# Performance work log

Hardware: AMD Instinct MI355X
Metric: run time of the kernel (lower is better)

Reference implementation:

```python
import jax, jax.numpy as jnp
import numpy as np

N_NODES = 100000


def _gcn_layer(x, W, b, src, dst, n):
    # PyG GCNConv: x' = D^-1/2 (A+I) D^-1/2 (x W) + b, with self-loops added.
    x = x @ W  # [N, out]
    loop = jnp.arange(n, dtype=src.dtype)
    src_f = jnp.concatenate([src, loop])
    dst_f = jnp.concatenate([dst, loop])
    deg = jax.ops.segment_sum(jnp.ones_like(dst_f, dtype=x.dtype), dst_f, num_segments=n)
    dinv = jnp.where(deg > 0, jax.lax.rsqrt(deg), 0.0)
    norm = dinv[src_f] * dinv[dst_f]  # [E+N]
    msgs = x[src_f] * norm[:, None]   # gather + scale
    out = jax.ops.segment_sum(msgs, dst_f, num_segments=n)
    return out + b


def setup_inputs() -> dict:
    key = jax.random.key(0)
    ks = jax.random.split(key, 16)
    inputFeatures = jax.random.normal(ks[0], (N_NODES, 64), dtype=jnp.float32)
    edge_index = jax.random.randint(ks[1], (2, 1000000), 0, N_NODES, dtype=jnp.int64)

    def lin(k, fan_in, fan_out):
        s = 1.0 / np.sqrt(fan_in)
        return jax.random.uniform(k, (fan_in, fan_out), jnp.float32, -s, s)

    return {
        "inputFeatures": inputFeatures,
        "W1": lin(ks[2], 64, 100), "b1": jnp.zeros((100,), jnp.float32),
        "W2": lin(ks[3], 100, 50), "b2": jnp.zeros((50,), jnp.float32),
        "W3": lin(ks[4], 50, 25), "b3": jnp.zeros((25,), jnp.float32),
        "Wl1": lin(ks[5], 25, 25), "bl1": jnp.zeros((25,), jnp.float32),
        "Wl2": lin(ks[6], 25, 10), "bl2": jnp.zeros((10,), jnp.float32),
        "Wl3": lin(ks[7], 10, 1), "bl3": jnp.zeros((1,), jnp.float32),
        "edge_index": edge_index,
    }


def reference(inputFeatures, W1, b1, W2, b2, W3, b3, Wl1, bl1, Wl2, bl2, Wl3, bl3, edge_index):
    src, dst = edge_index[0], edge_index[1]
    n = inputFeatures.shape[0]
    x = jax.nn.relu(_gcn_layer(inputFeatures, W1, b1, src, dst, n))
    x = jax.nn.relu(_gcn_layer(x, W2, b2, src, dst, n))
    x = jax.nn.relu(_gcn_layer(x, W3, b3, src, dst, n))
    x = jax.nn.relu(x @ Wl1 + bl1)
    x = jax.nn.relu(x @ Wl2 + bl2)
    x = jax.nn.relu(x @ Wl3 + bl3)
    return x  # [N, 1]
```

## Files before the change

kernel.cpp:

```cpp
#include <hip/hip_runtime.h>
#include <hip/hip_fp16.h>
#include <cstdint>

constexpr int BSHIFT = 9;
constexpr int NBUCK  = 256;
constexpr int BUCKET_CAP = 6144;

struct alignas(16) H8 { __half2 a, b, c, d; };
struct alignas(8)  H4 { __half2 a, b; };

typedef _Float16 f16x8 __attribute__((ext_vector_type(8)));
typedef float    f32x4 __attribute__((ext_vector_type(4)));

__device__ __forceinline__ float4 add4(float4 a, float4 b) {
    return make_float4(a.x + b.x, a.y + b.y, a.z + b.z, a.w + b.w);
}
__device__ __forceinline__ float4 mul4s(float4 a, float s) {
    return make_float4(a.x * s, a.y * s, a.z * s, a.w * s);
}
__device__ __forceinline__ void acc_h8(float4& A0, float4& A1, const H8 v, float s) {
    float2 f0 = __half22float2(v.a), f1 = __half22float2(v.b);
    float2 f2 = __half22float2(v.c), f3 = __half22float2(v.d);
    A0.x = fmaf(f0.x, s, A0.x); A0.y = fmaf(f0.y, s, A0.y);
    A0.z = fmaf(f1.x, s, A0.z); A0.w = fmaf(f1.y, s, A0.w);
    A1.x = fmaf(f2.x, s, A1.x); A1.y = fmaf(f2.y, s, A1.y);
    A1.z = fmaf(f3.x, s, A1.z); A1.w = fmaf(f3.y, s, A1.w);
}


constexpr int EPT = 16;
__global__ __launch_bounds__(256) void partition_edges(
    const int* __restrict__ src, const int* __restrict__ dst,
    int* __restrict__ bucketCur, int* __restrict__ pairs, int ne) {
    __shared__ int lcnt[NBUCK];
    __shared__ int lbase[NBUCK];
    int base = blockIdx.x * (256 * EPT);
    if (threadIdx.x < NBUCK) lcnt[threadIdx.x] = 0;
    __syncthreads();
    int2 ed[EPT];
    int  rnk[EPT];
#pragma unroll
    for (int j = 0; j < EPT; ++j) {
        int e = base + j * 256 + threadIdx.x;
        if (e < ne) {
            int d = dst[e];
            ed[j] = make_int2(src[e], d);
            rnk[j] = atomicAdd(&lcnt[d >> BSHIFT], 1);
        } else {
            ed[j].y = -1;
        }
    }
    __syncthreads();
    if (threadIdx.x < NBUCK) {
        int c = lcnt[threadIdx.x];
        lbase[threadIdx.x] = c ? atomicAdd(&bucketCur[threadIdx.x], c) : 0;
    }
    __syncthreads();
#pragma unroll
    for (int j = 0; j < EPT; ++j) {
        if (ed[j].y >= 0) {
            int b = ed[j].y >> BSHIFT;
            int p = lbase[b] + rnk[j];
            if (p < BUCKET_CAP)
                pairs[(size_t)b * BUCKET_CAP + p] =
                    (ed[j].x << BSHIFT) | (ed[j].y & ((1 << BSHIFT) - 1));
        }
    }
}

__global__ void scan_buckets(const int* __restrict__ bucketCnt, int* __restrict__ bucketBase,
                             int* __restrict__ offs, int n, int ne, int nbuckets) {
    __shared__ int tmp[256];
    int c = (threadIdx.x < (unsigned)nbuckets) ? bucketCnt[threadIdx.x] : 0;
    tmp[threadIdx.x] = c;
    __syncthreads();
    for (int off = 1; off < 256; off <<= 1) {
        int t = (threadIdx.x >= (unsigned)off) ? tmp[threadIdx.x - off] : 0;
        __syncthreads();
        tmp[threadIdx.x] += t;
        __syncthreads();
    }
    if (threadIdx.x < (unsigned)nbuckets) bucketBase[threadIdx.x] = tmp[threadIdx.x] - c;
    if (threadIdx.x == 0) offs[n] = ne;
}

__global__ __launch_bounds__(256) void bucket_csr(
    const int* __restrict__ pairs, const int* __restrict__ bucketCnt,
    const int* __restrict__ bucketBase, int* __restrict__ offs,
    float* __restrict__ dinv, int* __restrict__ csr, int n) {
    constexpr int BN = 1 << BSHIFT;
    __shared__ int hist[BN];
    __shared__ int cur[BN];
    __shared__ int tmp[256];
    int b = blockIdx.x;
    int cnt  = bucketCnt[b];
    int base = bucketBase[b];
    const int* pb = pairs + (size_t)b * BUCKET_CAP;
    int nodeLo = b << BSHIFT;

    hist[threadIdx.x] = 0;
    hist[threadIdx.x + 256] = 0;
    __syncthreads();
    for (int e = threadIdx.x; e < cnt; e += 256)
        atomicAdd(&hist[pb[e] & (BN - 1)], 1);
    __syncthreads();

    int l0 = 2 * threadIdx.x, l1 = l0 + 1;
    int h0 = hist[l0], h1 = hist[l1];
    tmp[threadIdx.x] = h0 + h1;
    __syncthreads();
    for (int off = 1; off < 256; off <<= 1) {
        int t = (threadIdx.x >= (unsigned)off) ? tmp[threadIdx.x - off] : 0;
        __syncthreads();
        tmp[threadIdx.x] += t;
        __syncthreads();
    }
    int e0 = tmp[threadIdx.x] - (h0 + h1);
    int e1 = e0 + h0;
    int g0 = nodeLo + l0, g1 = nodeLo + l1;
    if (g0 < n) { offs[g0] = base + e0; dinv[g0] = rsqrtf((float)(h0 + 1)); }
    if (g1 < n) { offs[g1] = base + e1; dinv[g1] = rsqrtf((float)(h1 + 1)); }
    cur[l0] = e0;
    cur[l1] = e1;
    __syncthreads();

    for (int e = threadIdx.x; e < cnt; e += 256) {
        int p = pb[e];
        int pos = atomicAdd(&cur[p & (BN - 1)], 1);
        csr[base + pos] = ((unsigned)p) >> BSHIFT;
    }
}

__global__ void pack_weights(const float* __restrict__ W1, const float* __restrict__ W2,
                             const float* __restrict__ W3,
                             __half* __restrict__ P1, __half* __restrict__ P2,
                             __half* __restrict__ P3) {
    int t = threadIdx.x;
    for (int i = t; i < 7 * 2 * 64 * 8; i += 256) {
        int j = i & 7, lane = (i >> 3) & 63, f = i >> 9;
        int mt = f >> 1, kf = f & 1;
        int k = kf * 32 + (lane >> 4) * 8 + j;
        int m = mt * 16 + (lane & 15);
        P1[i] = __float2half_rn(m < 100 ? W1[k * 100 + m] : 0.0f);
    }
    for (int i = t; i < 4 * 4 * 64 * 8; i += 256) {
        int j = i & 7, lane = (i >> 3) & 63, f = i >> 9;
        int mt = f >> 2, kf = f & 3;
        int k = kf * 32 + (lane >> 4) * 8 + j;
        int m = mt * 16 + (lane & 15);
        P2[i] = __float2half_rn((k < 100 && m < 50) ? W2[k * 50 + m] : 0.0f);
    }
    for (int i = t; i < 2 * 2 * 64 * 8; i += 256) {
        int j = i & 7, lane = (i >> 3) & 63, f = i >> 9;
        int mt = f >> 1, kf = f & 1;
        int k = kf * 32 + (lane >> 4) * 8 + j;
        int m = mt * 16 + (lane & 15);
        P3[i] = __float2half_rn((k < 50 && m < 25) ? W3[k * 25 + m] : 0.0f);
    }
}

__global__ void cvt_scale_f32_f16(const float* __restrict__ x, const float* __restrict__ dinv,
                                  __half* __restrict__ o, int n4) {
    int i = blockIdx.x * blockDim.x + threadIdx.x;
    if (i < n4) {
        float dv = dinv[i >> 4];
        float4 v = ((const float4*)x)[i];
        H4 h;
        h.a = __floats2half2_rn(v.x * dv, v.y * dv);
        h.b = __floats2half2_rn(v.z * dv, v.w * dv);
        ((H4*)o)[i] = h;
    }
}

__global__ __launch_bounds__(256) void agg1_h(
    const __half* __restrict__ s, const int* __restrict__ offs,
    const int* __restrict__ csr, const float* __restrict__ dinv,
    __half* __restrict__ out, int n) {
    int lane = threadIdx.x & 7;
    int node = blockIdx.x * 32 + (threadIdx.x >> 3);
    if (node >= n) return;
    int f0 = lane * 8;
    float dv = dinv[node];

    float4 z = make_float4(0.f, 0.f, 0.f, 0.f);
    float4 a00 = z, a01 = z, a10 = z, a11 = z, a20 = z, a21 = z, a30 = z, a31 = z;
    {
        H8 sv = *(const H8*)&s[(size_t)node * 64 + f0];
        acc_h8(a00, a01, sv, 1.0f);
    }
    int e0 = offs[node], e1 = offs[node + 1];
    int e = e0;
    for (; e + 4 <= e1; e += 4) {
        int i0 = csr[e], i1 = csr[e + 1], i2 = csr[e + 2], i3 = csr[e + 3];
        H8 v0 = *(const H8*)&s[(size_t)i0 * 64 + f0];
        H8 v1 = *(const H8*)&s[(size_t)i1 * 64 + f0];
        H8 v2 = *(const H8*)&s[(size_t)i2 * 64 + f0];
        H8 v3 = *(const H8*)&s[(size_t)i3 * 64 + f0];
        acc_h8(a00, a01, v0, 1.0f);
        acc_h8(a10, a11, v1, 1.0f);
        acc_h8(a20, a21, v2, 1.0f);
        acc_h8(a30, a31, v3, 1.0f);
    }
    for (; e < e1; ++e) {
        int sid = csr[e];
        H8 v = *(const H8*)&s[(size_t)sid * 64 + f0];
        acc_h8(a00, a01, v, 1.0f);
    }
    float4 A0 = add4(add4(a00, a10), add4(a20, a30));
    float4 A1 = add4(add4(a01, a11), add4(a21, a31));
    A0 = mul4s(A0, dv);
    A1 = mul4s(A1, dv);

    H8 h;
    h.a = __floats2half2_rn(A0.x, A0.y);
    h.b = __floats2half2_rn(A0.z, A0.w);
    h.c = __floats2half2_rn(A1.x, A1.y);
    h.d = __floats2half2_rn(A1.z, A1.w);
    *(H8*)&out[(size_t)node * 64 + f0] = h;
}

__global__ __launch_bounds__(256) void agg2_h16(
    const __half* __restrict__ s, const int* __restrict__ offs,
    const int* __restrict__ csr, const float* __restrict__ dinv,
    const float* __restrict__ b, __half* __restrict__ out, int n) {
    constexpr int MH = 50, SH = 64;
    int lane = threadIdx.x & 7;
    int node = blockIdx.x * 32 + (threadIdx.x >> 3);
    if (node >= n) return;
    int f0 = lane * 8;
    H8 zh{};
    if (f0 >= 56) {
        *(H8*)&out[(size_t)node * SH + f0] = zh;
        return;
    }
    float dv = dinv[node];

    float4 z = make_float4(0.f, 0.f, 0.f, 0.f);
    float4 a00 = z, a01 = z, a10 = z, a11 = z, a20 = z, a21 = z, a30 = z, a31 = z;
    {
        H8 sv = *(const H8*)&s[(size_t)node * SH + f0];
        acc_h8(a00, a01, sv, 1.0f);
    }
    int e0 = offs[node], e1 = offs[node + 1];
    int e = e0;
    for (; e + 4 <= e1; e += 4) {
        int i0 = csr[e], i1 = csr[e + 1], i2 = csr[e + 2], i3 = csr[e + 3];
        H8 v0 = *(const H8*)&s[(size_t)i0 * SH + f0];
        H8 v1 = *(const H8*)&s[(size_t)i1 * SH + f0];
        H8 v2 = *(const H8*)&s[(size_t)i2 * SH + f0];
        H8 v3 = *(const H8*)&s[(size_t)i3 * SH + f0];
        acc_h8(a00, a01, v0, 1.0f);
        acc_h8(a10, a11, v1, 1.0f);
        acc_h8(a20, a21, v2, 1.0f);
        acc_h8(a30, a31, v3, 1.0f);
    }
    for (; e < e1; ++e) {
        H8 v = *(const H8*)&s[(size_t)csr[e] * SH + f0];
        acc_h8(a00, a01, v, 1.0f);
    }
    float4 A0 = add4(add4(a00, a10), add4(a20, a30));
    float4 A1 = add4(add4(a01, a11), add4(a21, a31));
    float v[8] = {A0.x, A0.y, A0.z, A0.w, A1.x, A1.y, A1.z, A1.w};
#pragma unroll
    for (int i = 0; i < 8; ++i)
        v[i] = (f0 + i < MH) ? fmaxf(dv * v[i] + b[f0 + i], 0.0f) : 0.0f;
    H8 h;
    h.a = __floats2half2_rn(v[0], v[1]);
    h.b = __floats2half2_rn(v[2], v[3]);
    h.c = __floats2half2_rn(v[4], v[5]);
    h.d = __floats2half2_rn(v[6], v[7]);
    *(H8*)&out[(size_t)node * SH + f0] = h;
}

constexpr int HP = 136;
__global__ __launch_bounds__(256, 4) void gemm12_mfma(
    const __half* __restrict__ x, const __half* __restrict__ P1,
    const float* __restrict__ b1, const __half* __restrict__ P2,
    const float* __restrict__ dinv, __half* __restrict__ out, int n) {
    __shared__ _Float16 Hs[128 * HP];
    int tid = threadIdx.x;
    int lane = tid & 63;
    int w = tid >> 6;
    int lg = lane >> 4;
    int lr = lane & 15;
    int blockBase = blockIdx.x * 128;
    int waveBase  = blockBase + w * 32;

    for (int i = tid; i < 128 * 2; i += 256) {
        f16x8 zz = {};
        *(f16x8*)&Hs[(i >> 1) * HP + 112 + (i & 1) * 8] = zz;
    }

    float b1v[7];
#pragma unroll
    for (int mt = 0; mt < 7; ++mt) {
        int m = mt * 16 + lr;
        b1v[mt] = (m < 100) ? b1[m] : 0.0f;
    }

    const f16x8* P1v = (const f16x8*)P1;
#pragma unroll
    for (int rt = 0; rt < 2; ++rt) {
        int rowG = waveBase + rt * 16 + lr;
        f16x8 a0 = {}, a1 = {};
        if (rowG < n) {
            a0 = *(const f16x8*)&x[(size_t)rowG * 64 + lg * 8];
            a1 = *(const f16x8*)&x[(size_t)rowG * 64 + 32 + lg * 8];
        }
        int hbase = w * 32 + rt * 16;
#pragma unroll
        for (int mt = 0; mt < 7; ++mt) {
            f16x8 w0 = P1v[(mt * 2 + 0) * 64 + lane];
            f16x8 w1 = P1v[(mt * 2 + 1) * 64 + lane];
            f32x4 acc = {};
            acc = __builtin_amdgcn_mfma_f32_16x16x32_f16(a0, w0, acc, 0, 0, 0);
            acc = __builtin_amdgcn_mfma_f32_16x16x32_f16(a1, w1, acc, 0, 0, 0);
            int col = mt * 16 + lr;
#pragma unroll
            for (int i = 0; i < 4; ++i) {
                int rloc = hbase + lg * 4 + i;
                Hs[rloc * HP + col] = (_Float16)fmaxf(acc[i] + b1v[mt], 0.0f);
            }
        }
    }
    __syncthreads();

    const f16x8* P2v = (const f16x8*)P2;
#pragma unroll
    for (int mt = 0; mt < 4; ++mt) {
        f16x8 w0 = P2v[(mt * 4 + 0) * 64 + lane];
        f16x8 w1 = P2v[(mt * 4 + 1) * 64 + lane];
        f16x8 w2 = P2v[(mt * 4 + 2) * 64 + lane];
        f16x8 w3 = P2v[(mt * 4 + 3) * 64 + lane];
#pragma unroll
        for (int rt = 0; rt < 2; ++rt) {
            int lbase = w * 32 + rt * 16;
            const _Float16* hrow = &Hs[(size_t)(lbase + lr) * HP];
            f16x8 a0 = *(const f16x8*)&hrow[lg * 8];
            f16x8 a1 = *(const f16x8*)&hrow[32 + lg * 8];
            f16x8 a2 = *(const f16x8*)&hrow[64 + lg * 8];
            f16x8 a3 = *(const f16x8*)&hrow[96 + lg * 8];
            f32x4 acc = {};
            acc = __builtin_amdgcn_mfma_f32_16x16x32_f16(a0, w0, acc, 0, 0, 0);
            acc = __builtin_amdgcn_mfma_f32_16x16x32_f16(a1, w1, acc, 0, 0, 0);
            acc = __builtin_amdgcn_mfma_f32_16x16x32_f16(a2, w2, acc, 0, 0, 0);
            acc = __builtin_amdgcn_mfma_f32_16x16x32_f16(a3, w3, acc, 0, 0, 0);
            int col = mt * 16 + lr;
#pragma unroll
            for (int i = 0; i < 4; ++i) {
                int node = blockBase + lbase + lg * 4 + i;
                if (node < n)
                    out[(size_t)node * 64 + col] = __float2half_rn(acc[i] * dinv[node]);
            }
        }
    }
}

__global__ __launch_bounds__(256, 4) void gemm3_mfma(
    const __half* __restrict__ x, const __half* __restrict__ P3,
    const float* __restrict__ dinv, __half* __restrict__ out, int n) {
    int tid = threadIdx.x, lane = tid & 63, w = tid >> 6;
    int lg = lane >> 4, lr = lane & 15;
    int waveBase = blockIdx.x * 128 + w * 32;
    const f16x8* P3v = (const f16x8*)P3;
    f16x8 w00 = P3v[0 * 64 + lane], w01 = P3v[1 * 64 + lane];
    f16x8 w10 = P3v[2 * 64 + lane], w11 = P3v[3 * 64 + lane];
#pragma unroll
    for (int rt = 0; rt < 2; ++rt) {
        int rowG = waveBase + rt * 16 + lr;
        f16x8 a0 = {}, a1 = {};
        if (rowG < n) {
            a0 = *(const f16x8*)&x[(size_t)rowG * 64 + lg * 8];
            a1 = *(const f16x8*)&x[(size_t)rowG * 64 + 32 + lg * 8];
        }
#pragma unroll
        for (int mt = 0; mt < 2; ++mt) {
            f32x4 acc = {};
            acc = __builtin_amdgcn_mfma_f32_16x16x32_f16(a0, mt ? w10 : w00, acc, 0, 0, 0);
            acc = __builtin_amdgcn_mfma_f32_16x16x32_f16(a1, mt ? w11 : w01, acc, 0, 0, 0);
            int col = mt * 16 + lr;
#pragma unroll
            for (int i = 0; i < 4; ++i) {
                int node = waveBase + rt * 16 + lg * 4 + i;
                if (node < n)
                    out[(size_t)node * 32 + col] = __float2half_rn(acc[i] * dinv[node]);
            }
        }
    }
}

__global__ __launch_bounds__(256) void agg3_mlp_h(
    const __half* __restrict__ s, const int* __restrict__ offs,
    const int* __restrict__ csr, const float* __restrict__ dinv,
    const float* __restrict__ bg,
    const float* __restrict__ Wl1, const float* __restrict__ bl1,
    const float* __restrict__ Wl2, const float* __restrict__ bl2,
    const float* __restrict__ Wl3, const float* __restrict__ bl3,
    float* __restrict__ out, int n) {
    constexpr int MH = 25, SH = 32, LPN = 4;
    __shared__ float W1s[625], W2s[250], W3s[10], b1s[25], b2s[10];
    __shared__ float accs[64 * 26];
    __shared__ float b3s;

    for (int i = threadIdx.x; i < 625; i += 256) W1s[i] = Wl1[i];
    for (int i = threadIdx.x; i < 250; i += 256) W2s[i] = Wl2[i];
    if (threadIdx.x < 10) { W3s[threadIdx.x] = Wl3[threadIdx.x]; b2s[threadIdx.x] = bl2[threadIdx.x]; }
    if (threadIdx.x < 25) b1s[threadIdx.x] = bl1[threadIdx.x];
    if (threadIdx.x == 0) b3s = bl3[0];

    int lane = threadIdx.x % LPN;
    int nl   = threadIdx.x / LPN;
    int node = blockIdx.x * 64 + nl;
    int f0 = lane * 8;

    if (node < n && f0 < MH) {
        float dv = dinv[node];
        float4 z = make_float4(0.f, 0.f, 0.f, 0.f);
        float4 a00 = z, a01 = z, a10 = z, a11 = z, a20 = z, a21 = z, a30 = z, a31 = z;
        {
            H8 sv = *(const H8*)&s[(size_t)node * SH + f0];
            acc_h8(a00, a01, sv, 1.0f);
        }
        int e0 = offs[node], e1 = offs[node + 1];
        int e = e0;
        for (; e + 4 <= e1; e += 4) {
            int i0 = csr[e], i1 = csr[e + 1], i2 = csr[e + 2], i3 = csr[e + 3];
            H8 v0 = *(const H8*)&s[(size_t)i0 * SH + f0];
            H8 v1 = *(const H8*)&s[(size_t)i1 * SH + f0];
            H8 v2 = *(const H8*)&s[(size_t)i2 * SH + f0];
            H8 v3 = *(const H8*)&s[(size_t)i3 * SH + f0];
            acc_h8(a00, a01, v0, 1.0f);
            acc_h8(a10, a11, v1, 1.0f);
            acc_h8(a20, a21, v2, 1.0f);
            acc_h8(a30, a31, v3, 1.0f);
        }
        for (; e < e1; ++e) {
            H8 v = *(const H8*)&s[(size_t)csr[e] * SH + f0];
            acc_h8(a00, a01, v, 1.0f);
        }
        float4 A0 = add4(add4(a00, a10), add4(a20, a30));
        float4 A1 = add4(add4(a01, a11), add4(a21, a31));
        float v[8] = {A0.x, A0.y, A0.z, A0.w, A1.x, A1.y, A1.z, A1.w};
#pragma unroll
        for (int i = 0; i < 8; ++i)
            if (f0 + i < MH)
                accs[nl * 26 + f0 + i] = fmaxf(dv * v[i] + bg[f0 + i], 0.0f);
    }
    __syncthreads();

    if (threadIdx.x < 64) {
        int nd = blockIdx.x * 64 + threadIdx.x;
        if (nd < n) {
            const float* xr = &accs[threadIdx.x * 26];
            float h1[25];
#pragma unroll
            for (int m = 0; m < 25; ++m) {
                float a = b1s[m];
#pragma unroll
                for (int k = 0; k < 25; ++k) a = fmaf(xr[k], W1s[k * 25 + m], a);
                h1[m] = fmaxf(a, 0.0f);
            }
            float h2[10];
#pragma unroll
            for (int m = 0; m < 10; ++m) {
                float a = b2s[m];
#pragma unroll
                for (int k = 0; k < 25; ++k) a = fmaf(h1[k], W2s[k * 10 + m], a);
                h2[m] = fmaxf(a, 0.0f);
            }
            float a = b3s;
#pragma unroll
            for (int k = 0; k < 10; ++k) a = fmaf(h2[k], W3s[k], a);
            out[nd] = fmaxf(a, 0.0f);
        }
    }
}


extern "C" void kernel_launch(void* const* d_in, const int* in_sizes, int n_in,
                              void* d_out, int out_size, void* d_ws, size_t ws_size,
                              hipStream_t stream) {
    const float* x0  = (const float*)d_in[0];
    const float* W1  = (const float*)d_in[1];
    const float* b1  = (const float*)d_in[2];
    const float* W2  = (const float*)d_in[3];
    const float* b2  = (const float*)d_in[4];
    const float* W3  = (const float*)d_in[5];
    const float* b3  = (const float*)d_in[6];
    const float* Wl1 = (const float*)d_in[7];
    const float* bl1 = (const float*)d_in[8];
    const float* Wl2 = (const float*)d_in[9];
    const float* bl2 = (const float*)d_in[10];
    const float* Wl3 = (const float*)d_in[11];
    const float* bl3 = (const float*)d_in[12];
    const int*   edge = (const int*)d_in[13];

    int n  = in_sizes[0] / 64;
    int ne = in_sizes[13] / 2;
    const int* esrc = edge;
    const int* edst = edge + ne;

    char* ws = (char*)d_ws;
    auto alloc = [&](size_t bytes) {
        char* p = ws;
        ws += (bytes + 255) & ~(size_t)255;
        return p;
    };
    int*    offs       = (int*)alloc((size_t)(n + 1) * 4);
    int*    bucketCur  = (int*)alloc(NBUCK * 4);
    int*    bucketBase = (int*)alloc(NBUCK * 4);
    int*    csr        = (int*)alloc((size_t)ne * 4);
    float*  dinv       = (float*)alloc((size_t)n * 4);
    __half* x0h        = (__half*)alloc((size_t)n * 64 * 2);
    __half* bufAh      = (__half*)alloc((size_t)n * 64 * 2);
    __half* bufDh      = (__half*)alloc((size_t)n * 64 * 2);
    __half* P1         = (__half*)alloc(7 * 2 * 64 * 8 * 2);
    __half* P2         = (__half*)alloc(4 * 4 * 64 * 8 * 2);
    __half* P3         = (__half*)alloc(2 * 2 * 64 * 8 * 2);
    int*    pairs = (int*)bufDh;
    __half* bufEh = x0h;
    __half* bufCh = bufAh;
    (void)ws_size; (void)n_in; (void)out_size;

    int nbuckets = (n + (1 << BSHIFT) - 1) >> BSHIFT;

    pack_weights<<<1, 256, 0, stream>>>(W1, W2, W3, P1, P2, P3);

    hipMemsetAsync(bucketCur, 0, NBUCK * 4, stream);
    partition_edges<<<(ne + 256 * EPT - 1) / (256 * EPT), 256, 0, stream>>>(
        esrc, edst, bucketCur, pairs, ne);
    scan_buckets<<<1, 256, 0, stream>>>(bucketCur, bucketBase, offs, n, ne, nbuckets);
    bucket_csr<<<nbuckets, 256, 0, stream>>>(pairs, bucketCur, bucketBase, offs, dinv, csr, n);

    cvt_scale_f32_f16<<<(n * 16 + 255) / 256, 256, 0, stream>>>(x0, dinv, x0h, n * 16);

    agg1_h<<<(n + 31) / 32, 256, 0, stream>>>(x0h, offs, csr, dinv, bufAh, n);

    gemm12_mfma<<<(n + 127) / 128, 256, 0, stream>>>(bufAh, P1, b1, P2, dinv, bufDh, n);

    agg2_h16<<<(n + 31) / 32, 256, 0, stream>>>(bufDh, offs, csr, dinv, b2, bufEh, n);

    gemm3_mfma<<<(n + 127) / 128, 256, 0, stream>>>(bufEh, P3, dinv, bufCh, n);

    agg3_mlp_h<<<(n + 63) / 64, 256, 0, stream>>>(
        bufCh, offs, csr, dinv, b3, Wl1, bl1, Wl2, bl2, Wl3, bl3, (float*)d_out, n);
}
```

Before: 253.3 us.

## Fuse aggregation with following MFMA GEMMs and merge preprocessing kernels

Fuses layer-1 aggregation with the two-stage MFMA GEMM (agg1gemm12) and layer-2 aggregation with the layer-3 GEMM (agg2g3), staging aggregated rows in LDS instead of writing and re-reading them from global memory. Weight packing moves into an extra block of the edge-partition kernel, and the bucket prefix scan is recomputed redundantly inside every bucket_csr block. Together these remove three launches and two intermediate global round-trips. The cost is smaller GEMM tiles per block (64 or 32 rows instead of 128), more LDS per block, and gather and MFMA phases serialized within each block.

```diff
diff --git a/kernel.cpp b/kernel.cpp
--- a/kernel.cpp
+++ b/kernel.cpp
@@ -29,9 +29,37 @@
 
 
 constexpr int EPT = 16;
-__global__ __launch_bounds__(256) void partition_edges(
+__global__ __launch_bounds__(256) void partition_pack(
     const int* __restrict__ src, const int* __restrict__ dst,
-    int* __restrict__ bucketCur, int* __restrict__ pairs, int ne) {
+    int* __restrict__ bucketCur, int* __restrict__ pairs, int ne, int nEdgeBlocks,
+    const float* __restrict__ W1, const float* __restrict__ W2,
+    const float* __restrict__ W3,
+    __half* __restrict__ P1, __half* __restrict__ P2, __half* __restrict__ P3) {
+    if (blockIdx.x == (unsigned)nEdgeBlocks) {
+        int t = threadIdx.x;
+        for (int i = t; i < 7 * 2 * 64 * 8; i += 256) {
+            int j = i & 7, lane = (i >> 3) & 63, f = i >> 9;
+            int mt = f >> 1, kf = f & 1;
+            int k = kf * 32 + (lane >> 4) * 8 + j;
+            int m = mt * 16 + (lane & 15);
+            P1[i] = __float2half_rn(m < 100 ? W1[k * 100 + m] : 0.0f);
+        }
+        for (int i = t; i < 4 * 4 * 64 * 8; i += 256) {
+            int j = i & 7, lane = (i >> 3) & 63, f = i >> 9;
+            int mt = f >> 2, kf = f & 3;
+            int k = kf * 32 + (lane >> 4) * 8 + j;
+            int m = mt * 16 + (lane & 15);
+            P2[i] = __float2half_rn((k < 100 && m < 50) ? W2[k * 50 + m] : 0.0f);
+        }
+        for (int i = t; i < 2 * 2 * 64 * 8; i += 256) {
+            int j = i & 7, lane = (i >> 3) & 63, f = i >> 9;
+            int mt = f >> 1, kf = f & 1;
+            int k = kf * 32 + (lane >> 4) * 8 + j;
+            int m = mt * 16 + (lane & 15);
+            P3[i] = __float2half_rn((k < 50 && m < 25) ? W3[k * 25 + m] : 0.0f);
+        }
+        return;
+    }
     __shared__ int lcnt[NBUCK];
     __shared__ int lbase[NBUCK];
     int base = blockIdx.x * (256 * EPT);
@@ -68,54 +96,55 @@
     }
 }
 
-__global__ void scan_buckets(const int* __restrict__ bucketCnt, int* __restrict__ bucketBase,
-                             int* __restrict__ offs, int n, int ne, int nbuckets) {
-    __shared__ int tmp[256];
-    int c = (threadIdx.x < (unsigned)nbuckets) ? bucketCnt[threadIdx.x] : 0;
-    tmp[threadIdx.x] = c;
-    __syncthreads();
-    for (int off = 1; off < 256; off <<= 1) {
-        int t = (threadIdx.x >= (unsigned)off) ? tmp[threadIdx.x - off] : 0;
-        __syncthreads();
-        tmp[threadIdx.x] += t;
-        __syncthreads();
-    }
-    if (threadIdx.x < (unsigned)nbuckets) bucketBase[threadIdx.x] = tmp[threadIdx.x] - c;
-    if (threadIdx.x == 0) offs[n] = ne;
-}
-
-__global__ __launch_bounds__(256) void bucket_csr(
+__global__ __launch_bounds__(256) void bucket_csr_scan(
     const int* __restrict__ pairs, const int* __restrict__ bucketCnt,
-    const int* __restrict__ bucketBase, int* __restrict__ offs,
-    float* __restrict__ dinv, int* __restrict__ csr, int n) {
+    int* __restrict__ offs, float* __restrict__ dinv, int* __restrict__ csr,
+    int n, int ne, int nbuckets) {
     constexpr int BN = 1 << BSHIFT;
     __shared__ int hist[BN];
     __shared__ int cur[BN];
     __shared__ int tmp[256];
+    __shared__ int baseS;
     int b = blockIdx.x;
+    int t = threadIdx.x;
+
+    int c = (t < (unsigned)nbuckets) ? bucketCnt[t] : 0;
+    tmp[t] = c;
+    __syncthreads();
+    for (int off = 1; off < 256; off <<= 1) {
+        int v = (t >= (unsigned)off) ? tmp[t - off] : 0;
+        __syncthreads();
+        tmp[t] += v;
+        __syncthreads();
+    }
+    if (t == 0) {
+        baseS = b ? tmp[b - 1] : 0;
+        if (b == 0) offs[n] = ne;
+    }
+    __syncthreads();
+    int base = baseS;
     int cnt  = bucketCnt[b];
-    int base = bucketBase[b];
     const int* pb = pairs + (size_t)b * BUCKET_CAP;
     int nodeLo = b << BSHIFT;
 
-    hist[threadIdx.x] = 0;
-    hist[threadIdx.x + 256] = 0;
-    __syncthreads();
-    for (int e = threadIdx.x; e < cnt; e += 256)
+    hist[t] = 0;
+    hist[t + 256] = 0;
+    __syncthreads();
+    for (int e = t; e < cnt; e += 256)
         atomicAdd(&hist[pb[e] & (BN - 1)], 1);
     __syncthreads();
 
-    int l0 = 2 * threadIdx.x, l1 = l0 + 1;
+    int l0 = 2 * t, l1 = l0 + 1;
     int h0 = hist[l0], h1 = hist[l1];
-    tmp[threadIdx.x] = h0 + h1;
+    tmp[t] = h0 + h1;
     __syncthreads();
     for (int off = 1; off < 256; off <<= 1) {
-        int t = (threadIdx.x >= (unsigned)off) ? tmp[threadIdx.x - off] : 0;
+        int v = (t >= (unsigned)off) ? tmp[t - off] : 0;
         __syncthreads();
-        tmp[threadIdx.x] += t;
+        tmp[t] += v;
         __syncthreads();
     }
-    int e0 = tmp[threadIdx.x] - (h0 + h1);
+    int e0 = tmp[t] - (h0 + h1);
     int e1 = e0 + h0;
     int g0 = nodeLo + l0, g1 = nodeLo + l1;
     if (g0 < n) { offs[g0] = base + e0; dinv[g0] = rsqrtf((float)(h0 + 1)); }
@@ -124,38 +153,10 @@
     cur[l1] = e1;
     __syncthreads();
 
-    for (int e = threadIdx.x; e < cnt; e += 256) {
+    for (int e = t; e < cnt; e += 256) {
         int p = pb[e];
         int pos = atomicAdd(&cur[p & (BN - 1)], 1);
         csr[base + pos] = ((unsigned)p) >> BSHIFT;
-    }
-}
-
-__global__ void pack_weights(const float* __restrict__ W1, const float* __restrict__ W2,
-                             const float* __restrict__ W3,
-                             __half* __restrict__ P1, __half* __restrict__ P2,
-                             __half* __restrict__ P3) {
-    int t = threadIdx.x;
-    for (int i = t; i < 7 * 2 * 64 * 8; i += 256) {
-        int j = i & 7, lane = (i >> 3) & 63, f = i >> 9;
-        int mt = f >> 1, kf = f & 1;
-        int k = kf * 32 + (lane >> 4) * 8 + j;
-        int m = mt * 16 + (lane & 15);
-        P1[i] = __float2half_rn(m < 100 ? W1[k * 100 + m] : 0.0f);
-    }
-    for (int i = t; i < 4 * 4 * 64 * 8; i += 256) {
-        int j = i & 7, lane = (i >> 3) & 63, f = i >> 9;
-        int mt = f >> 2, kf = f & 3;
-        int k = kf * 32 + (lane >> 4) * 8 + j;
-        int m = mt * 16 + (lane & 15);
-        P2[i] = __float2half_rn((k < 100 && m < 50) ? W2[k * 50 + m] : 0.0f);
-    }
-    for (int i = t; i < 2 * 2 * 64 * 8; i += 256) {
-        int j = i & 7, lane = (i >> 3) & 63, f = i >> 9;
-        int mt = f >> 1, kf = f & 1;
-        int k = kf * 32 + (lane >> 4) * 8 + j;
-        int m = mt * 16 + (lane & 15);
-        P3[i] = __float2half_rn((k < 50 && m < 25) ? W3[k * 25 + m] : 0.0f);
     }
 }
 
@@ -172,142 +173,79 @@
     }
 }
 
-__global__ __launch_bounds__(256) void agg1_h(
-    const __half* __restrict__ s, const int* __restrict__ offs,
+constexpr int XSP = 72;
+constexpr int HPS = 136;
+__global__ __launch_bounds__(256, 4) void agg1gemm12(
+    const __half* __restrict__ x, const int* __restrict__ offs,
     const int* __restrict__ csr, const float* __restrict__ dinv,
-    __half* __restrict__ out, int n) {
-    int lane = threadIdx.x & 7;
-    int node = blockIdx.x * 32 + (threadIdx.x >> 3);
-    if (node >= n) return;
-    int f0 = lane * 8;
-    float dv = dinv[node];
-
-    float4 z = make_float4(0.f, 0.f, 0.f, 0.f);
-    float4 a00 = z, a01 = z, a10 = z, a11 = z, a20 = z, a21 = z, a30 = z, a31 = z;
-    {
-        H8 sv = *(const H8*)&s[(size_t)node * 64 + f0];
-        acc_h8(a00, a01, sv, 1.0f);
-    }
-    int e0 = offs[node], e1 = offs[node + 1];
-    int e = e0;
-    for (; e + 4 <= e1; e += 4) {
-        int i0 = csr[e], i1 = csr[e + 1], i2 = csr[e + 2], i3 = csr[e + 3];
-        H8 v0 = *(const H8*)&s[(size_t)i0 * 64 + f0];
-        H8 v1 = *(const H8*)&s[(size_t)i1 * 64 + f0];
-        H8 v2 = *(const H8*)&s[(size_t)i2 * 64 + f0];
-        H8 v3 = *(const H8*)&s[(size_t)i3 * 64 + f0];
-        acc_h8(a00, a01, v0, 1.0f);
-        acc_h8(a10, a11, v1, 1.0f);
-        acc_h8(a20, a21, v2, 1.0f);
-        acc_h8(a30, a31, v3, 1.0f);
-    }
-    for (; e < e1; ++e) {
-        int sid = csr[e];
-        H8 v = *(const H8*)&s[(size_t)sid * 64 + f0];
-        acc_h8(a00, a01, v, 1.0f);
-    }
-    float4 A0 = add4(add4(a00, a10), add4(a20, a30));
-    float4 A1 = add4(add4(a01, a11), add4(a21, a31));
-    A0 = mul4s(A0, dv);
-    A1 = mul4s(A1, dv);
-
-    H8 h;
-    h.a = __floats2half2_rn(A0.x, A0.y);
-    h.b = __floats2half2_rn(A0.z, A0.w);
-    h.c = __floats2half2_rn(A1.x, A1.y);
-    h.d = __floats2half2_rn(A1.z, A1.w);
-    *(H8*)&out[(size_t)node * 64 + f0] = h;
-}
-
-__global__ __launch_bounds__(256) void agg2_h16(
-    const __half* __restrict__ s, const int* __restrict__ offs,
-    const int* __restrict__ csr, const float* __restrict__ dinv,
-    const float* __restrict__ b, __half* __restrict__ out, int n) {
-    constexpr int MH = 50, SH = 64;
-    int lane = threadIdx.x & 7;
-    int node = blockIdx.x * 32 + (threadIdx.x >> 3);
-    if (node >= n) return;
-    int f0 = lane * 8;
-    H8 zh{};
-    if (f0 >= 56) {
-        *(H8*)&out[(size_t)node * SH + f0] = zh;
-        return;
-    }
-    float dv = dinv[node];
-
-    float4 z = make_float4(0.f, 0.f, 0.f, 0.f);
-    float4 a00 = z, a01 = z, a10 = z, a11 = z, a20 = z, a21 = z, a30 = z, a31 = z;
-    {
-        H8 sv = *(const H8*)&s[(size_t)node * SH + f0];
-        acc_h8(a00, a01, sv, 1.0f);
-    }
-    int e0 = offs[node], e1 = offs[node + 1];
-    int e = e0;
-    for (; e + 4 <= e1; e += 4) {
-        int i0 = csr[e], i1 = csr[e + 1], i2 = csr[e + 2], i3 = csr[e + 3];
-        H8 v0 = *(const H8*)&s[(size_t)i0 * SH + f0];
-        H8 v1 = *(const H8*)&s[(size_t)i1 * SH + f0];
-        H8 v2 = *(const H8*)&s[(size_t)i2 * SH + f0];
-        H8 v3 = *(const H8*)&s[(size_t)i3 * SH + f0];
-        acc_h8(a00, a01, v0, 1.0f);
-        acc_h8(a10, a11, v1, 1.0f);
-        acc_h8(a20, a21, v2, 1.0f);
-        acc_h8(a30, a31, v3, 1.0f);
-    }
-    for (; e < e1; ++e) {
-        H8 v = *(const H8*)&s[(size_t)csr[e] * SH + f0];
-        acc_h8(a00, a01, v, 1.0f);
-    }
-    float4 A0 = add4(add4(a00, a10), add4(a20, a30));
-    float4 A1 = add4(add4(a01, a11), add4(a21, a31));
-    float v[8] = {A0.x, A0.y, A0.z, A0.w, A1.x, A1.y, A1.z, A1.w};
-#pragma unroll
-    for (int i = 0; i < 8; ++i)
-        v[i] = (f0 + i < MH) ? fmaxf(dv * v[i] + b[f0 + i], 0.0f) : 0.0f;
-    H8 h;
-    h.a = __floats2half2_rn(v[0], v[1]);
-    h.b = __floats2half2_rn(v[2], v[3]);
-    h.c = __floats2half2_rn(v[4], v[5]);
-    h.d = __floats2half2_rn(v[6], v[7]);
-    *(H8*)&out[(size_t)node * SH + f0] = h;
-}
-
-constexpr int HP = 136;
-__global__ __launch_bounds__(256, 4) void gemm12_mfma(
-    const __half* __restrict__ x, const __half* __restrict__ P1,
-    const float* __restrict__ b1, const __half* __restrict__ P2,
-    const float* __restrict__ dinv, __half* __restrict__ out, int n) {
-    __shared__ _Float16 Hs[128 * HP];
-    int tid = threadIdx.x;
-    int lane = tid & 63;
-    int w = tid >> 6;
-    int lg = lane >> 4;
-    int lr = lane & 15;
-    int blockBase = blockIdx.x * 128;
-    int waveBase  = blockBase + w * 32;
-
-    for (int i = tid; i < 128 * 2; i += 256) {
+    const __half* __restrict__ P1, const float* __restrict__ b1,
+    const __half* __restrict__ P2, __half* __restrict__ out, int n) {
+    __shared__ alignas(16) _Float16 Xs[64 * XSP];
+    __shared__ alignas(16) _Float16 Hs[64 * HPS];
+    int tid = threadIdx.x, lane = tid & 63, w = tid >> 6;
+    int lg = lane >> 4, lr = lane & 15;
+    int blockBase = blockIdx.x * 64;
+
+    for (int i = tid; i < 64 * 2; i += 256) {
         f16x8 zz = {};
-        *(f16x8*)&Hs[(i >> 1) * HP + 112 + (i & 1) * 8] = zz;
-    }
-
+        *(f16x8*)&Hs[(i >> 1) * HPS + 112 + (i & 1) * 8] = zz;
+    }
+
+    int f0 = (lane & 7) * 8;
+#pragma unroll
+    for (int p = 0; p < 2; ++p) {
+        int nl = w * 16 + p * 8 + (lane >> 3);
+        int node = blockBase + nl;
+        float4 z4 = make_float4(0.f, 0.f, 0.f, 0.f);
+        float4 a00 = z4, a01 = z4, a10 = z4, a11 = z4, a20 = z4, a21 = z4, a30 = z4, a31 = z4;
+        float dv = 0.0f;
+        if (node < n) {
+            dv = dinv[node];
+            H8 sv = *(const H8*)&x[(size_t)node * 64 + f0];
+            acc_h8(a00, a01, sv, 1.0f);
+            int e0 = offs[node], e1 = offs[node + 1];
+            int e = e0;
+            for (; e + 4 <= e1; e += 4) {
+                int i0 = csr[e], i1 = csr[e + 1], i2 = csr[e + 2], i3 = csr[e + 3];
+                H8 v0 = *(const H8*)&x[(size_t)i0 * 64 + f0];
+                H8 v1 = *(const H8*)&x[(size_t)i1 * 64 + f0];
+                H8 v2 = *(const H8*)&x[(size_t)i2 * 64 + f0];
+                H8 v3 = *(const H8*)&x[(size_t)i3 * 64 + f0];
+                acc_h8(a00, a01, v0, 1.0f);
+                acc_h8(a10, a11, v1, 1.0f);
+                acc_h8(a20, a21, v2, 1.0f);
+                acc_h8(a30, a31, v3, 1.0f);
+            }
+            for (; e < e1; ++e) {
+                H8 v = *(const H8*)&x[(size_t)csr[e] * 64 + f0];
+                acc_h8(a00, a01, v, 1.0f);
+            }
+        }
+        float4 A0 = add4(add4(a00, a10), add4(a20, a30));
+        float4 A1 = add4(add4(a01, a11), add4(a21, a31));
+        A0 = mul4s(A0, dv);
+        A1 = mul4s(A1, dv);
+        H8 h;
+        h.a = __floats2half2_rn(A0.x, A0.y);
+        h.b = __floats2half2_rn(A0.z, A0.w);
+        h.c = __floats2half2_rn(A1.x, A1.y);
+        h.d = __floats2half2_rn(A1.z, A1.w);
+        *(H8*)&Xs[nl * XSP + f0] = h;
+    }
+    __syncthreads();
+
+    const f16x8* P1v = (const f16x8*)P1;
     float b1v[7];
 #pragma unroll
     for (int mt = 0; mt < 7; ++mt) {
         int m = mt * 16 + lr;
         b1v[mt] = (m < 100) ? b1[m] : 0.0f;
     }
-
-    const f16x8* P1v = (const f16x8*)P1;
-#pragma unroll
-    for (int rt = 0; rt < 2; ++rt) {
-        int rowG = waveBase + rt * 16 + lr;
-        f16x8 a0 = {}, a1 = {};
-        if (rowG < n) {
-            a0 = *(const f16x8*)&x[(size_t)rowG * 64 + lg * 8];
-            a1 = *(const f16x8*)&x[(size_t)rowG * 64 + 32 + lg * 8];
-        }
-        int hbase = w * 32 + rt * 16;
+    {
+        int rowL = w * 16 + lr;
+        f16x8 a0 = *(const f16x8*)&Xs[rowL * XSP + lg * 8];
+        f16x8 a1 = *(const f16x8*)&Xs[rowL * XSP + 32 + lg * 8];
+        int hbase = w * 16;
 #pragma unroll
         for (int mt = 0; mt < 7; ++mt) {
             f16x8 w0 = P1v[(mt * 2 + 0) * 64 + lane];
@@ -319,7 +257,7 @@
 #pragma unroll
             for (int i = 0; i < 4; ++i) {
                 int rloc = hbase + lg * 4 + i;
-                Hs[rloc * HP + col] = (_Float16)fmaxf(acc[i] + b1v[mt], 0.0f);
+                Hs[rloc * HPS + col] = (_Float16)fmaxf(acc[i] + b1v[mt], 0.0f);
             }
         }
     }
@@ -332,60 +270,101 @@
         f16x8 w1 = P2v[(mt * 4 + 1) * 64 + lane];
         f16x8 w2 = P2v[(mt * 4 + 2) * 64 + lane];
         f16x8 w3 = P2v[(mt * 4 + 3) * 64 + lane];
-#pragma unroll
-        for (int rt = 0; rt < 2; ++rt) {
-            int lbase = w * 32 + rt * 16;
-            const _Float16* hrow = &Hs[(size_t)(lbase + lr) * HP];
-            f16x8 a0 = *(const f16x8*)&hrow[lg * 8];
-            f16x8 a1 = *(const f16x8*)&hrow[32 + lg * 8];
-            f16x8 a2 = *(const f16x8*)&hrow[64 + lg * 8];
-            f16x8 a3 = *(const f16x8*)&hrow[96 + lg * 8];
-            f32x4 acc = {};
-            acc = __builtin_amdgcn_mfma_f32_16x16x32_f16(a0, w0, acc, 0, 0, 0);
-            acc = __builtin_amdgcn_mfma_f32_16x16x32_f16(a1, w1, acc, 0, 0, 0);
-            acc = __builtin_amdgcn_mfma_f32_16x16x32_f16(a2, w2, acc, 0, 0, 0);
-            acc = __builtin_amdgcn_mfma_f32_16x16x32_f16(a3, w3, acc, 0, 0, 0);
-            int col = mt * 16 + lr;
-#pragma unroll
-            for (int i = 0; i < 4; ++i) {
-                int node = blockBase + lbase + lg * 4 + i;
-                if (node < n)
-                    out[(size_t)node * 64 + col] = __float2half_rn(acc[i] * dinv[node]);
-            }
-        }
-    }
-}
-
-__global__ __launch_bounds__(256, 4) void gemm3_mfma(
-    const __half* __restrict__ x, const __half* __restrict__ P3,
-    const float* __restrict__ dinv, __half* __restrict__ out, int n) {
+        int lbase = w * 16;
+        const _Float16* hrow = &Hs[(size_t)(lbase + lr) * HPS];
+        f16x8 a0 = *(const f16x8*)&hrow[lg * 8];
+        f16x8 a1 = *(const f16x8*)&hrow[32 + lg * 8];
+        f16x8 a2 = *(const f16x8*)&hrow[64 + lg * 8];
+        f16x8 a3 = *(const f16x8*)&hrow[96 + lg * 8];
+        f32x4 acc = {};
+        acc = __builtin_amdgcn_mfma_f32_16x16x32_f16(a0, w0, acc, 0, 0, 0);
+        acc = __builtin_amdgcn_mfma_f32_16x16x32_f16(a1, w1, acc, 0, 0, 0);
+        acc = __builtin_amdgcn_mfma_f32_16x16x32_f16(a2, w2, acc, 0, 0, 0);
+        acc = __builtin_amdgcn_mfma_f32_16x16x32_f16(a3, w3, acc, 0, 0, 0);
+        int col = mt * 16 + lr;
+#pragma unroll
+        for (int i = 0; i < 4; ++i) {
+            int node = blockBase + lbase + lg * 4 + i;
+            if (node < n)
+                out[(size_t)node * 64 + col] = __float2half_rn(acc[i] * dinv[node]);
+        }
+    }
+}
+
+constexpr int YP = 72;
+__global__ __launch_bounds__(256) void agg2g3(
+    const __half* __restrict__ s, const int* __restrict__ offs,
+    const int* __restrict__ csr, const float* __restrict__ dinv,
+    const float* __restrict__ b2, const __half* __restrict__ P3,
+    __half* __restrict__ out, int n) {
+    constexpr int MH = 50, SH = 64;
+    __shared__ alignas(16) _Float16 Ys[32 * YP];
     int tid = threadIdx.x, lane = tid & 63, w = tid >> 6;
     int lg = lane >> 4, lr = lane & 15;
-    int waveBase = blockIdx.x * 128 + w * 32;
+    int blockBase = blockIdx.x * 32;
+
+    int nodeL = tid >> 3;
+    int f0 = (tid & 7) * 8;
+    int node = blockBase + nodeL;
+    float v[8] = {0.f, 0.f, 0.f, 0.f, 0.f, 0.f, 0.f, 0.f};
+    if (node < n && f0 < 56) {
+        float dv = dinv[node];
+        float4 z4 = make_float4(0.f, 0.f, 0.f, 0.f);
+        float4 a00 = z4, a01 = z4, a10 = z4, a11 = z4, a20 = z4, a21 = z4, a30 = z4, a31 = z4;
+        {
+            H8 sv = *(const H8*)&s[(size_t)node * SH + f0];
+            acc_h8(a00, a01, sv, 1.0f);
+        }
+        int e0 = offs[node], e1 = offs[node + 1];
+        int e = e0;
+        for (; e + 4 <= e1; e += 4) {
+            int i0 = csr[e], i1 = csr[e + 1], i2 = csr[e + 2], i3 = csr[e + 3];
+            H8 v0 = *(const H8*)&s[(size_t)i0 * SH + f0];
+            H8 v1 = *(const H8*)&s[(size_t)i1 * SH + f0];
+            H8 v2 = *(const H8*)&s[(size_t)i2 * SH + f0];
+            H8 v3 = *(const H8*)&s[(size_t)i3 * SH + f0];
+            acc_h8(a00, a01, v0, 1.0f);
+            acc_h8(a10, a11, v1, 1.0f);
+            acc_h8(a20, a21, v2, 1.0f);
+            acc_h8(a30, a31, v3, 1.0f);
+        }
+        for (; e < e1; ++e) {
+            H8 vv = *(const H8*)&s[(size_t)csr[e] * SH + f0];
+            acc_h8(a00, a01, vv, 1.0f);
+        }
+        float4 A0 = add4(add4(a00, a10), add4(a20, a30));
+        float4 A1 = add4(add4(a01, a11), add4(a21, a31));
+        float vr[8] = {A0.x, A0.y, A0.z, A0.w, A1.x, A1.y, A1.z, A1.w};
+#pragma unroll
+        for (int i = 0; i < 8; ++i)
+            v[i] = (f0 + i < MH) ? fmaxf(dv * vr[i] + b2[f0 + i], 0.0f) : 0.0f;
+    }
+    {
+        H8 h;
+        h.a = __floats2half2_rn(v[0], v[1]);
+        h.b = __floats2half2_rn(v[2], v[3]);
+        h.c = __floats2half2_rn(v[4], v[5]);
+        h.d = __floats2half2_rn(v[6], v[7]);
+        *(H8*)&Ys[nodeL * YP + f0] = h;
+    }
+    __syncthreads();
+
+    int rt = w >> 1, mt = w & 1;
     const f16x8* P3v = (const f16x8*)P3;
-    f16x8 w00 = P3v[0 * 64 + lane], w01 = P3v[1 * 64 + lane];
-    f16x8 w10 = P3v[2 * 64 + lane], w11 = P3v[3 * 64 + lane];
-#pragma unroll
-    for (int rt = 0; rt < 2; ++rt) {
-        int rowG = waveBase + rt * 16 + lr;
-        f16x8 a0 = {}, a1 = {};
-        if (rowG < n) {
-            a0 = *(const f16x8*)&x[(size_t)rowG * 64 + lg * 8];
-            a1 = *(const f16x8*)&x[(size_t)rowG * 64 + 32 + lg * 8];
-        }
-#pragma unroll
-        for (int mt = 0; mt < 2; ++mt) {
-            f32x4 acc = {};
-            acc = __builtin_amdgcn_mfma_f32_16x16x32_f16(a0, mt ? w10 : w00, acc, 0, 0, 0);
-            acc = __builtin_amdgcn_mfma_f32_16x16x32_f16(a1, mt ? w11 : w01, acc, 0, 0, 0);
-            int col = mt * 16 + lr;
-#pragma unroll
-            for (int i = 0; i < 4; ++i) {
-                int node = waveBase + rt * 16 + lg * 4 + i;
-                if (node < n)
-                    out[(size_t)node * 32 + col] = __float2half_rn(acc[i] * dinv[node]);
-            }
-        }
+    f16x8 w0 = P3v[(mt * 2 + 0) * 64 + lane];
+    f16x8 w1 = P3v[(mt * 2 + 1) * 64 + lane];
+    int rowL = rt * 16 + lr;
+    f16x8 a0 = *(const f16x8*)&Ys[rowL * YP + lg * 8];
+    f16x8 a1 = *(const f16x8*)&Ys[rowL * YP + 32 + lg * 8];
+    f32x4 acc = {};
+    acc = __builtin_amdgcn_mfma_f32_16x16x32_f16(a0, w0, acc, 0, 0, 0);
+    acc = __builtin_amdgcn_mfma_f32_16x16x32_f16(a1, w1, acc, 0, 0, 0);
+    int col = mt * 16 + lr;
+#pragma unroll
+    for (int i = 0; i < 4; ++i) {
+        int nd = blockBase + rt * 16 + lg * 4 + i;
+        if (nd < n)
+            out[(size_t)nd * 32 + col] = __float2half_rn(acc[i] * dinv[nd]);
     }
 }
 
@@ -508,39 +487,33 @@
     };
     int*    offs       = (int*)alloc((size_t)(n + 1) * 4);
     int*    bucketCur  = (int*)alloc(NBUCK * 4);
-    int*    bucketBase = (int*)alloc(NBUCK * 4);
     int*    csr        = (int*)alloc((size_t)ne * 4);
     float*  dinv       = (float*)alloc((size_t)n * 4);
     __half* x0h        = (__half*)alloc((size_t)n * 64 * 2);
-    __half* bufAh      = (__half*)alloc((size_t)n * 64 * 2);
     __half* bufDh      = (__half*)alloc((size_t)n * 64 * 2);
+    __half* bufCh      = (__half*)alloc((size_t)n * 32 * 2);
     __half* P1         = (__half*)alloc(7 * 2 * 64 * 8 * 2);
     __half* P2         = (__half*)alloc(4 * 4 * 64 * 8 * 2);
     __half* P3         = (__half*)alloc(2 * 2 * 64 * 8 * 2);
     int*    pairs = (int*)bufDh;
-    __half* bufEh = x0h;
-    __half* bufCh = bufAh;
     (void)ws_size; (void)n_in; (void)out_size;
 
     int nbuckets = (n + (1 << BSHIFT) - 1) >> BSHIFT;
-
-    pack_weights<<<1, 256, 0, stream>>>(W1, W2, W3, P1, P2, P3);
+    int nchunk   = (ne + 256 * EPT - 1) / (256 * EPT);
 
     hipMemsetAsync(bucketCur, 0, NBUCK * 4, stream);
-    partition_edges<<<(ne + 256 * EPT - 1) / (256 * EPT), 256, 0, stream>>>(
-        esrc, edst, bucketCur, pairs, ne);
-    scan_buckets<<<1, 256, 0, stream>>>(bucketCur, bucketBase, offs, n, ne, nbuckets);
-    bucket_csr<<<nbuckets, 256, 0, stream>>>(pairs, bucketCur, bucketBase, offs, dinv, csr, n);
+    partition_pack<<<nchunk + 1, 256, 0, stream>>>(
+        esrc, edst, bucketCur, pairs, ne, nchunk, W1, W2, W3, P1, P2, P3);
+    bucket_csr_scan<<<nbuckets, 256, 0, stream>>>(
+        pairs, bucketCur, offs, dinv, csr, n, ne, nbuckets);
 
     cvt_scale_f32_f16<<<(n * 16 + 255) / 256, 256, 0, stream>>>(x0, dinv, x0h, n * 16);
 
-    agg1_h<<<(n + 31) / 32, 256, 0, stream>>>(x0h, offs, csr, dinv, bufAh, n);
-
-    gemm12_mfma<<<(n + 127) / 128, 256, 0, stream>>>(bufAh, P1, b1, P2, dinv, bufDh, n);
-
-    agg2_h16<<<(n + 31) / 32, 256, 0, stream>>>(bufDh, offs, csr, dinv, b2, bufEh, n);
-
-    gemm3_mfma<<<(n + 127) / 128, 256, 0, stream>>>(bufEh, P3, dinv, bufCh, n);
+    agg1gemm12<<<(n + 63) / 64, 256, 0, stream>>>(
+        x0h, offs, csr, dinv, P1, b1, P2, bufDh, n);
+
+    agg2g3<<<(n + 31) / 32, 256, 0, stream>>>(
+        bufDh, offs, csr, dinv, b2, P3, bufCh, n);
 
     agg3_mlp_h<<<(n + 63) / 64, 256, 0, stream>>>(
         bufCh, offs, csr, dinv, b3, Wl1, bl1, Wl2, bl2, Wl3, bl3, (float*)d_out, n);
```

Measured after the change: 230.8 us. 1.1x faster.
